# Kernel optimization log

Measured on AMD Instinct MI355X. Metric: run time of the kernel, lower is better.

Reference implementation:

```python
import jax, jax.numpy as jnp
import numpy as np

N, FIN, FOUT, H = 6144, 128, 64, 2
ALPHA = 0.2      # leaky relu slope
EPS = 1e-5       # layernorm eps
NEG = -9e15      # mask value from original code


def setup_inputs() -> dict:
    key = jax.random.key(0)
    k1, k2, k3, k4 = jax.random.split(key, 4)
    h = jax.random.normal(k1, (N, FIN), dtype=jnp.float32)
    adj = jax.random.randint(k2, (N, N), 0, 2, dtype=jnp.int32)
    # xavier_uniform over (fan_in, fan_out) of last two dims
    limW = float(np.sqrt(6.0 / (FIN + FOUT)))
    W = jax.random.uniform(k3, (H, FIN, FOUT), jnp.float32, -limW, limW)
    lima = float(np.sqrt(6.0 / (2 * FOUT + 1)))
    a = jax.random.uniform(k4, (H, 2 * FOUT, 1), jnp.float32, -lima, lima)
    gamma = jnp.ones((H * FOUT,), jnp.float32)
    beta = jnp.zeros((H * FOUT,), jnp.float32)
    return {"h": h, "adj": adj, "W": W, "a": a, "gamma": gamma, "beta": beta}


def reference(h, adj, W, a, gamma, beta):
    # h: [N, Fin], adj: [N, N] int, W: [H, Fin, Fout], a: [H, 2*Fout, 1]
    ht = jnp.einsum('ni,hio->hno', h, W)          # [H, N, Fout]
    a1 = a[:, :FOUT, 0]                            # [H, Fout]
    a2 = a[:, FOUT:, 0]                            # [H, Fout]
    # concat score a^T [h_i || h_j] == s1_i + s2_j (identical math, no NxNx2F tensor)
    s1 = jnp.einsum('hno,ho->hn', ht, a1)          # [H, N]
    s2 = jnp.einsum('hno,ho->hn', ht, a2)          # [H, N]
    e = s1[:, :, None] + s2[:, None, :]            # [H, N, N]
    e = jnp.where(e > 0, e, ALPHA * e)             # LeakyReLU
    e = jnp.where((adj > 0)[None], e, NEG)         # adjacency mask
    att = jax.nn.softmax(e, axis=-1)               # softmax over neighbors (dim=1 of [N,N])
    # dropout is identity in eval mode
    hp = jnp.einsum('hnm,hmo->hno', att, ht)       # [H, N, Fout]
    out = jnp.transpose(hp, (1, 0, 2)).reshape(N, H * FOUT)  # concat heads
    # LayerNorm(H*Fout), elementwise affine
    mu = out.mean(-1, keepdims=True)
    var = ((out - mu) ** 2).mean(-1, keepdims=True)
    out = (out - mu) / jnp.sqrt(var + EPS) * gamma + beta
    return out, att
```

## Files before the change

### kernel.cpp

```cpp
#include <hip/hip_runtime.h>
#include <hip/hip_bf16.h>

#define NNODES 6144
#define FIN    128
#define FOUTC  64
#define NHEAD  2
#define ALPHA  0.2f
#define LN_EPS 1e-5f
#define MASKW  192

typedef __attribute__((ext_vector_type(4))) float f32x4;
typedef __attribute__((ext_vector_type(8))) short short8;
typedef __attribute__((ext_vector_type(4))) int   i32x4;

static __device__ __forceinline__ short f2bf(float x) {
    unsigned u = __float_as_uint(x);
    u = (u + 0x7fffu + ((u >> 16) & 1u)) >> 16;
    return (short)u;
}

static __device__ __forceinline__ short f2bf_hw(float x) {
    return (short)__bfloat16_as_ushort(__float2bfloat16(x));
}

static __device__ __forceinline__ float pcalc(float s1v, float s2v, unsigned bit,
                                              bool uni, float inv) {
    float e = s1v + s2v;
    e = fmaxf(e, ALPHA * e);
    float t = bit ? __expf(e) : 0.0f;
    t = uni ? 1.0f : t;
    return t * inv;
}

static __device__ __forceinline__ float ecalc(float s1v, float s2v, int am) {
    float e = s1v + s2v;
    e = fmaxf(e, ALPHA * e);
    return (am > 0) ? __expf(e) : 0.0f;
}

static __device__ __forceinline__ float tcalc(float s1v, float s2v, unsigned bit,
                                              bool uni) {
    float e = s1v + s2v;
    e = fmaxf(e, ALPHA * e);
    float t = bit ? __expf(e) : 0.0f;
    return uni ? 1.0f : t;
}

__global__ __launch_bounds__(256) void gat_k1(const float* __restrict__ h,
        const float* __restrict__ W, const float* __restrict__ a,
        short* __restrict__ htbP, float* __restrict__ s1, float* __restrict__ s2) {
    __shared__ float hrow[4][FIN];
    const int wid = threadIdx.x >> 6, lane = threadIdx.x & 63;
    const int n = blockIdx.x * 4 + wid;
    hrow[wid][lane]      = h[(size_t)n * FIN + lane];
    hrow[wid][lane + 64] = h[(size_t)n * FIN + lane + 64];
    __syncthreads();
    float acc0 = 0.f, acc1 = 0.f;
    #pragma unroll 8
    for (int k = 0; k < FIN; ++k) {
        float hv = hrow[wid][k];
        acc0 = fmaf(hv, W[k * FOUTC + lane], acc0);
        acc1 = fmaf(hv, W[(FIN + k) * FOUTC + lane], acc1);
    }
    const int it_ = n >> 5, kk = n & 31;
    const int fl  = (lane & 15) + ((kk >> 3) << 4);
    const size_t pb = ((size_t)(it_ * 4 + (lane >> 4))) * 512 + fl * 8 + (kk & 7);
    htbP[pb]          = f2bf(acc0);
    htbP[393216 + pb] = f2bf(acc1);
    float r00 = acc0 * a[lane];
    float r01 = acc0 * a[FOUTC + lane];
    float r10 = acc1 * a[2 * FOUTC + lane];
    float r11 = acc1 * a[3 * FOUTC + lane];
    #pragma unroll
    for (int off = 32; off; off >>= 1) {
        r00 += __shfl_xor(r00, off);
        r01 += __shfl_xor(r01, off);
        r10 += __shfl_xor(r10, off);
        r11 += __shfl_xor(r11, off);
    }
    if (lane == 0) {
        s1[n] = r00;          s2[n] = r01;
        s1[NNODES + n] = r10; s2[NNODES + n] = r11;
    }
}

__global__ __launch_bounds__(256) void gat_k2a(const int* __restrict__ adj,
        const float* __restrict__ s1, const float* __restrict__ s2,
        float* __restrict__ psum, unsigned* __restrict__ mask32) {
    const int n = blockIdx.x;
    const int t = threadIdx.x;
    const int wid = t >> 6, lane = t & 63;
    const i32x4* arow = (const i32x4*)(adj + (size_t)n * NNODES);
    const float4* s2h0 = (const float4*)(s2);
    const float4* s2h1 = (const float4*)(s2 + NNODES);
    const float s10 = s1[n], s11 = s1[NNODES + n];
    float sum0 = 0.f, sum1 = 0.f;
    unsigned* mrow = mask32 + (size_t)n * MASKW;
    #pragma unroll
    for (int i = 0; i < 6; ++i) {
        int c4 = t + i * 256;
        i32x4 av = __builtin_nontemporal_load(arow + c4);
        float4 sa = s2h0[c4];
        float4 sb = s2h1[c4];
        sum0 += (ecalc(s10, sa.x, av[0]) + ecalc(s10, sa.y, av[1]))
              + (ecalc(s10, sa.z, av[2]) + ecalc(s10, sa.w, av[3]));
        sum1 += (ecalc(s11, sb.x, av[0]) + ecalc(s11, sb.y, av[1]))
              + (ecalc(s11, sb.z, av[2]) + ecalc(s11, sb.w, av[3]));
        unsigned nib = (unsigned)(av[0] > 0) | ((unsigned)(av[1] > 0) << 1)
                     | ((unsigned)(av[2] > 0) << 2) | ((unsigned)(av[3] > 0) << 3);
        unsigned v = nib << ((lane & 7) * 4);
        v |= (unsigned)__shfl_xor((int)v, 1);
        v |= (unsigned)__shfl_xor((int)v, 2);
        v |= (unsigned)__shfl_xor((int)v, 4);
        if ((lane & 7) == 0)
            mrow[i * 32 + wid * 8 + (lane >> 3)] = v;
    }
    #pragma unroll
    for (int off = 32; off; off >>= 1) {
        sum0 += __shfl_xor(sum0, off);
        sum1 += __shfl_xor(sum1, off);
    }
    __shared__ float red[2][4];
    if (lane == 0) { red[0][wid] = sum0; red[1][wid] = sum1; }
    __syncthreads();
    if (t == 0) {
        psum[n]          = (red[0][0] + red[0][1]) + (red[0][2] + red[0][3]);
        psum[NNODES + n] = (red[1][0] + red[1][1]) + (red[1][2] + red[1][3]);
    }
}

template <int ITERS, int RATIO>
__global__ __launch_bounds__(256) void gat_mixed(const unsigned* __restrict__ mask32,
        const short* __restrict__ htbP, const float* __restrict__ s1,
        const float* __restrict__ s2, const float* __restrict__ psum,
        float* __restrict__ att, float* __restrict__ hpp) {
    const int bid = blockIdx.x;
    const int mid = bid / RATIO, rem = bid % RATIO;

    if (rem == RATIO - 1) {
        const int bx = (6144 / ITERS / 32 == 4) ? (mid & 1) : 0;
        const int by = (6144 / ITERS / 32 == 4) ? (mid >> 1) : mid;
        const int w = threadIdx.x >> 6, lane = threadIdx.x & 63;
        const int hh = w & 1, cs = w >> 1;
        const int pc = bx * 2 + cs;
        const int n0 = by * 16;
        const int r = lane & 15, g = lane >> 4;
        const int node = n0 + r;
        const float s1v = s1[hh * NNODES + node];
        const float ps  = psum[hh * NNODES + node];
        const bool uni = !(ps > 0.f);
        const float* s2h = s2 + hh * NNODES;
        const unsigned* mrow = mask32 + (size_t)node * MASKW + pc * ITERS;
        const short* bb = htbP + (size_t)(hh * 192 + pc * ITERS) * 2048 + (size_t)lane * 8;
        const int cbase = pc * ITERS * 32;

        f32x4 acc0 = {0.f,0.f,0.f,0.f}, acc1 = {0.f,0.f,0.f,0.f};
        f32x4 acc2 = {0.f,0.f,0.f,0.f}, acc3 = {0.f,0.f,0.f,0.f};

        #pragma unroll 4
        for (int it = 0; it < ITERS; ++it) {
            const int kb = cbase + it * 32 + g * 8;
            const unsigned mb = (mrow[it] >> (g * 8)) & 0xffu;
            float4 sa = *(const float4*)(s2h + kb);
            float4 sb = *(const float4*)(s2h + kb + 4);
            float t0 = tcalc(s1v, sa.x, mb & 1u,   uni);
            float t1 = tcalc(s1v, sa.y, mb & 2u,   uni);
            float t2 = tcalc(s1v, sa.z, mb & 4u,   uni);
            float t3 = tcalc(s1v, sa.w, mb & 8u,   uni);
            float t4 = tcalc(s1v, sb.x, mb & 16u,  uni);
            float t5 = tcalc(s1v, sb.y, mb & 32u,  uni);
            float t6 = tcalc(s1v, sb.z, mb & 64u,  uni);
            float t7 = tcalc(s1v, sb.w, mb & 128u, uni);
            short8 af = { f2bf_hw(t0), f2bf_hw(t1), f2bf_hw(t2), f2bf_hw(t3),
                          f2bf_hw(t4), f2bf_hw(t5), f2bf_hw(t6), f2bf_hw(t7) };
            const short* bp = bb + (size_t)it * 2048;
            short8 b0 = *(const short8*)(bp);
            short8 b1 = *(const short8*)(bp + 512);
            short8 b2 = *(const short8*)(bp + 1024);
            short8 b3 = *(const short8*)(bp + 1536);
            acc0 = __builtin_amdgcn_mfma_f32_16x16x32_bf16(af, b0, acc0, 0, 0, 0);
            acc1 = __builtin_amdgcn_mfma_f32_16x16x32_bf16(af, b1, acc1, 0, 0, 0);
            acc2 = __builtin_amdgcn_mfma_f32_16x16x32_bf16(af, b2, acc2, 0, 0, 0);
            acc3 = __builtin_amdgcn_mfma_f32_16x16x32_bf16(af, b3, acc3, 0, 0, 0);
        }
        float invO[4];
        #pragma unroll
        for (int reg = 0; reg < 4; ++reg) {
            float pso = psum[hh * NNODES + n0 + g * 4 + reg];
            invO[reg] = (pso > 0.f) ? (1.0f / pso) : (1.0f / (float)NNODES);
        }
        float* hb = hpp + ((size_t)(pc * NHEAD + hh) * NNODES + (n0 + g * 4)) * FOUTC + r;
        #pragma unroll
        for (int reg = 0; reg < 4; ++reg) {
            hb[(size_t)reg * FOUTC +  0] = acc0[reg] * invO[reg];
            hb[(size_t)reg * FOUTC + 16] = acc1[reg] * invO[reg];
            hb[(size_t)reg * FOUTC + 32] = acc2[reg] * invO[reg];
            hb[(size_t)reg * FOUTC + 48] = acc3[reg] * invO[reg];
        }
    } else {
        const int row = mid * (RATIO - 1) + rem;
        const int t = threadIdx.x;
        const float ps0 = psum[row],          ps1 = psum[NNODES + row];
        const bool u0 = !(ps0 > 0.f),         u1 = !(ps1 > 0.f);
        const float in0 = u0 ? (1.0f / (float)NNODES) : 1.0f / ps0;
        const float in1 = u1 ? (1.0f / (float)NNODES) : 1.0f / ps1;
        const float s10 = s1[row], s11 = s1[NNODES + row];
        const unsigned* mrow = mask32 + (size_t)row * MASKW;
        float* attr0 = att + (size_t)row * NNODES;
        float* attr1 = attr0 + (size_t)NNODES * NNODES;
        const int sh = (t & 7) * 4;
        #pragma unroll
        for (int i = 0; i < 6; ++i) {
            const int c0 = i * 1024 + t * 4;
            const unsigned bits = (mrow[c0 >> 5] >> sh) & 0xfu;
            float4 sv0 = *(const float4*)(s2 + c0);
            float4 sv1 = *(const float4*)(s2 + NNODES + c0);
            f32x4 st0 = { pcalc(s10, sv0.x, bits & 1u, u0, in0),
                          pcalc(s10, sv0.y, bits & 2u, u0, in0),
                          pcalc(s10, sv0.z, bits & 4u, u0, in0),
                          pcalc(s10, sv0.w, bits & 8u, u0, in0) };
            f32x4 st1 = { pcalc(s11, sv1.x, bits & 1u, u1, in1),
                          pcalc(s11, sv1.y, bits & 2u, u1, in1),
                          pcalc(s11, sv1.z, bits & 4u, u1, in1),
                          pcalc(s11, sv1.w, bits & 8u, u1, in1) };
            __builtin_nontemporal_store(st0, (f32x4*)(attr0 + c0));
            __builtin_nontemporal_store(st1, (f32x4*)(attr1 + c0));
        }
    }
}

__global__ __launch_bounds__(256) void gat_k4(const float* __restrict__ hpp,
        const float* __restrict__ gamma, const float* __restrict__ beta,
        float* __restrict__ out, int nchunk) {
    const int wid = threadIdx.x >> 6, lane = threadIdx.x & 63;
    const int n = blockIdx.x * 4 + wid;
    float v0 = 0.f, v1 = 0.f;
    for (int p = 0; p < nchunk; ++p) {
        v0 += hpp[((size_t)(p * NHEAD + 0) * NNODES + n) * FOUTC + lane];
        v1 += hpp[((size_t)(p * NHEAD + 1) * NNODES + n) * FOUTC + lane];
    }
    float s = v0 + v1;
    #pragma unroll
    for (int off = 32; off; off >>= 1) s += __shfl_xor(s, off);
    const float mu = s * (1.0f / 128.0f);
    const float d0 = v0 - mu, d1 = v1 - mu;
    float q = d0 * d0 + d1 * d1;
    #pragma unroll
    for (int off = 32; off; off >>= 1) q += __shfl_xor(q, off);
    const float rstd = 1.0f / sqrtf(q * (1.0f / 128.0f) + LN_EPS);
    out[(size_t)n * 128 + lane]      = d0 * rstd * gamma[lane] + beta[lane];
    out[(size_t)n * 128 + 64 + lane] = d1 * rstd * gamma[64 + lane] + beta[64 + lane];
}

extern "C" void kernel_launch(void* const* d_in, const int* in_sizes, int n_in,
                              void* d_out, int out_size, void* d_ws, size_t ws_size,
                              hipStream_t stream) {
    const float* h     = (const float*)d_in[0];
    const int*   adj   = (const int*)d_in[1];
    const float* W     = (const float*)d_in[2];
    const float* a     = (const float*)d_in[3];
    const float* gamma = (const float*)d_in[4];
    const float* beta  = (const float*)d_in[5];
    float* out = (float*)d_out;
    float* att = out + (size_t)NNODES * (NHEAD * FOUTC);

    char* ws = (char*)d_ws;
    short* htbP = (short*)ws;
    float* s1   = (float*)(ws + 1572864);
    float* s2p  = (float*)(ws + 1572864 + 49152);
    float* psum = (float*)(ws + 1572864 + 2 * 49152);
    unsigned* mask32 = (unsigned*)(ws + 1572864 + 3 * 49152);
    char* hpp_base = ws + 1572864 + 3 * 49152 + 4718592;
    size_t avail = (ws_size > 6438912) ? ws_size - 6438912 : 0;
    const size_t per_chunk = (size_t)NHEAD * NNODES * FOUTC * 4;
    const int nchunk = (avail >= 4 * per_chunk) ? 4 : 2;
    float* hpp = (float*)hpp_base;

    gat_k1<<<NNODES / 4, 256, 0, stream>>>(h, W, a, htbP, s1, s2p);
    gat_k2a<<<NNODES, 256, 0, stream>>>(adj, s1, s2p, psum, mask32);
    if (nchunk == 4) {
        gat_mixed<48, 9><<<6912, 256, 0, stream>>>(mask32, htbP, s1, s2p, psum, att, hpp);
    } else {
        gat_mixed<96, 17><<<6528, 256, 0, stream>>>(mask32, htbP, s1, s2p, psum, att, hpp);
    }
    gat_k4<<<NNODES / 4, 256, 0, stream>>>(hpp, gamma, beta, out, nchunk);
}
```

Measured before the change: 139.0 us.

## Fold softmax normalization into exp2 exponent and split attention rows per head

Scores are pre-scaled by log2(e) so exp2 can be used directly, and the 1/sum normalization is folded into the exponent as -log2(psum). The MFMA path now accumulates already-normalized probabilities, so the output rescale loop is removed. Attention-writer blocks now handle one head-row each instead of both heads, which doubles the grid and changes RATIO. Fully masked rows take a fast path that just stores the uniform value. Normalizing inside the exponent changes bf16 rounding of the MFMA operands slightly.

Measured after the change: 140.0 us. No clear change (+0.7%).

```diff
diff --git a/kernel.cpp b/kernel.cpp
--- a/kernel.cpp
+++ b/kernel.cpp
@@ -8,6 +8,8 @@
 #define ALPHA  0.2f
 #define LN_EPS 1e-5f
 #define MASKW  192
+#define LOG2E  1.4426950408889634f
+#define INVN   (1.0f / 6144.0f)
 
 typedef __attribute__((ext_vector_type(4))) float f32x4;
 typedef __attribute__((ext_vector_type(8))) short short8;
@@ -23,27 +25,15 @@
     return (short)__bfloat16_as_ushort(__float2bfloat16(x));
 }
 
-static __device__ __forceinline__ float pcalc(float s1v, float s2v, unsigned bit,
-                                              bool uni, float inv) {
-    float e = s1v + s2v;
-    e = fmaxf(e, ALPHA * e);
-    float t = bit ? __expf(e) : 0.0f;
-    t = uni ? 1.0f : t;
-    return t * inv;
-}
-
-static __device__ __forceinline__ float ecalc(float s1v, float s2v, int am) {
-    float e = s1v + s2v;
-    e = fmaxf(e, ALPHA * e);
-    return (am > 0) ? __expf(e) : 0.0f;
-}
-
-static __device__ __forceinline__ float tcalc(float s1v, float s2v, unsigned bit,
-                                              bool uni) {
-    float e = s1v + s2v;
-    e = fmaxf(e, ALPHA * e);
-    float t = bit ? __expf(e) : 0.0f;
-    return uni ? 1.0f : t;
+static __device__ __forceinline__ float ecalc2(float e, unsigned bit) {
+    float m = fmaxf(e, ALPHA * e);
+    return bit ? __builtin_amdgcn_exp2f(m) : 0.0f;
+}
+static __device__ __forceinline__ float pcalc2(float e, float li, unsigned bit,
+                                               bool uni) {
+    float m = fmaxf(e, ALPHA * e) + li;
+    float t = bit ? __builtin_amdgcn_exp2f(m) : 0.0f;
+    return uni ? INVN : t;
 }
 
 __global__ __launch_bounds__(256) void gat_k1(const float* __restrict__ h,
@@ -79,8 +69,8 @@
         r11 += __shfl_xor(r11, off);
     }
     if (lane == 0) {
-        s1[n] = r00;          s2[n] = r01;
-        s1[NNODES + n] = r10; s2[NNODES + n] = r11;
+        s1[n] = r00 * LOG2E;          s2[n] = r01 * LOG2E;
+        s1[NNODES + n] = r10 * LOG2E; s2[NNODES + n] = r11 * LOG2E;
     }
 }
 
@@ -102,12 +92,12 @@
         i32x4 av = __builtin_nontemporal_load(arow + c4);
         float4 sa = s2h0[c4];
         float4 sb = s2h1[c4];
-        sum0 += (ecalc(s10, sa.x, av[0]) + ecalc(s10, sa.y, av[1]))
-              + (ecalc(s10, sa.z, av[2]) + ecalc(s10, sa.w, av[3]));
-        sum1 += (ecalc(s11, sb.x, av[0]) + ecalc(s11, sb.y, av[1]))
-              + (ecalc(s11, sb.z, av[2]) + ecalc(s11, sb.w, av[3]));
         unsigned nib = (unsigned)(av[0] > 0) | ((unsigned)(av[1] > 0) << 1)
                      | ((unsigned)(av[2] > 0) << 2) | ((unsigned)(av[3] > 0) << 3);
+        sum0 += (ecalc2(s10 + sa.x, nib & 1u) + ecalc2(s10 + sa.y, nib & 2u))
+              + (ecalc2(s10 + sa.z, nib & 4u) + ecalc2(s10 + sa.w, nib & 8u));
+        sum1 += (ecalc2(s11 + sb.x, nib & 1u) + ecalc2(s11 + sb.y, nib & 2u))
+              + (ecalc2(s11 + sb.z, nib & 4u) + ecalc2(s11 + sb.w, nib & 8u));
         unsigned v = nib << ((lane & 7) * 4);
         v |= (unsigned)__shfl_xor((int)v, 1);
         v |= (unsigned)__shfl_xor((int)v, 2);
@@ -149,6 +139,7 @@
         const float s1v = s1[hh * NNODES + node];
         const float ps  = psum[hh * NNODES + node];
         const bool uni = !(ps > 0.f);
+        const float li = uni ? 0.f : -__log2f(ps);
         const float* s2h = s2 + hh * NNODES;
         const unsigned* mrow = mask32 + (size_t)node * MASKW + pc * ITERS;
         const short* bb = htbP + (size_t)(hh * 192 + pc * ITERS) * 2048 + (size_t)lane * 8;
@@ -163,16 +154,16 @@
             const unsigned mb = (mrow[it] >> (g * 8)) & 0xffu;
             float4 sa = *(const float4*)(s2h + kb);
             float4 sb = *(const float4*)(s2h + kb + 4);
-            float t0 = tcalc(s1v, sa.x, mb & 1u,   uni);
-            float t1 = tcalc(s1v, sa.y, mb & 2u,   uni);
-            float t2 = tcalc(s1v, sa.z, mb & 4u,   uni);
-            float t3 = tcalc(s1v, sa.w, mb & 8u,   uni);
-            float t4 = tcalc(s1v, sb.x, mb & 16u,  uni);
-            float t5 = tcalc(s1v, sb.y, mb & 32u,  uni);
-            float t6 = tcalc(s1v, sb.z, mb & 64u,  uni);
-            float t7 = tcalc(s1v, sb.w, mb & 128u, uni);
-            short8 af = { f2bf_hw(t0), f2bf_hw(t1), f2bf_hw(t2), f2bf_hw(t3),
-                          f2bf_hw(t4), f2bf_hw(t5), f2bf_hw(t6), f2bf_hw(t7) };
+            float p0 = pcalc2(s1v + sa.x, li, mb & 1u,   uni);
+            float p1 = pcalc2(s1v + sa.y, li, mb & 2u,   uni);
+            float p2 = pcalc2(s1v + sa.z, li, mb & 4u,   uni);
+            float p3 = pcalc2(s1v + sa.w, li, mb & 8u,   uni);
+            float p4 = pcalc2(s1v + sb.x, li, mb & 16u,  uni);
+            float p5 = pcalc2(s1v + sb.y, li, mb & 32u,  uni);
+            float p6 = pcalc2(s1v + sb.z, li, mb & 64u,  uni);
+            float p7 = pcalc2(s1v + sb.w, li, mb & 128u, uni);
+            short8 af = { f2bf_hw(p0), f2bf_hw(p1), f2bf_hw(p2), f2bf_hw(p3),
+                          f2bf_hw(p4), f2bf_hw(p5), f2bf_hw(p6), f2bf_hw(p7) };
             const short* bp = bb + (size_t)it * 2048;
             short8 b0 = *(const short8*)(bp);
             short8 b1 = *(const short8*)(bp + 512);
@@ -183,48 +174,43 @@
             acc2 = __builtin_amdgcn_mfma_f32_16x16x32_bf16(af, b2, acc2, 0, 0, 0);
             acc3 = __builtin_amdgcn_mfma_f32_16x16x32_bf16(af, b3, acc3, 0, 0, 0);
         }
-        float invO[4];
-        #pragma unroll
-        for (int reg = 0; reg < 4; ++reg) {
-            float pso = psum[hh * NNODES + n0 + g * 4 + reg];
-            invO[reg] = (pso > 0.f) ? (1.0f / pso) : (1.0f / (float)NNODES);
-        }
         float* hb = hpp + ((size_t)(pc * NHEAD + hh) * NNODES + (n0 + g * 4)) * FOUTC + r;
         #pragma unroll
         for (int reg = 0; reg < 4; ++reg) {
-            hb[(size_t)reg * FOUTC +  0] = acc0[reg] * invO[reg];
-            hb[(size_t)reg * FOUTC + 16] = acc1[reg] * invO[reg];
-            hb[(size_t)reg * FOUTC + 32] = acc2[reg] * invO[reg];
-            hb[(size_t)reg * FOUTC + 48] = acc3[reg] * invO[reg];
+            hb[(size_t)reg * FOUTC +  0] = acc0[reg];
+            hb[(size_t)reg * FOUTC + 16] = acc1[reg];
+            hb[(size_t)reg * FOUTC + 32] = acc2[reg];
+            hb[(size_t)reg * FOUTC + 48] = acc3[reg];
         }
     } else {
-        const int row = mid * (RATIO - 1) + rem;
+        const int idx = mid * (RATIO - 1) + rem;
+        const int hh  = idx / NNODES;
+        const int row = idx - hh * NNODES;
         const int t = threadIdx.x;
-        const float ps0 = psum[row],          ps1 = psum[NNODES + row];
-        const bool u0 = !(ps0 > 0.f),         u1 = !(ps1 > 0.f);
-        const float in0 = u0 ? (1.0f / (float)NNODES) : 1.0f / ps0;
-        const float in1 = u1 ? (1.0f / (float)NNODES) : 1.0f / ps1;
-        const float s10 = s1[row], s11 = s1[NNODES + row];
+        const float ps = psum[hh * NNODES + row];
+        float* attrow = att + ((size_t)hh * NNODES + row) * NNODES;
+        if (!(ps > 0.f)) {
+            const f32x4 u = {INVN, INVN, INVN, INVN};
+            #pragma unroll
+            for (int i = 0; i < 6; ++i)
+                __builtin_nontemporal_store(u, (f32x4*)(attrow + i * 1024 + t * 4));
+            return;
+        }
+        const float li = -__log2f(ps);
+        const float s1v = s1[hh * NNODES + row];
+        const float* s2h = s2 + hh * NNODES;
         const unsigned* mrow = mask32 + (size_t)row * MASKW;
-        float* attr0 = att + (size_t)row * NNODES;
-        float* attr1 = attr0 + (size_t)NNODES * NNODES;
         const int sh = (t & 7) * 4;
         #pragma unroll
         for (int i = 0; i < 6; ++i) {
             const int c0 = i * 1024 + t * 4;
             const unsigned bits = (mrow[c0 >> 5] >> sh) & 0xfu;
-            float4 sv0 = *(const float4*)(s2 + c0);
-            float4 sv1 = *(const float4*)(s2 + NNODES + c0);
-            f32x4 st0 = { pcalc(s10, sv0.x, bits & 1u, u0, in0),
-                          pcalc(s10, sv0.y, bits & 2u, u0, in0),
-                          pcalc(s10, sv0.z, bits & 4u, u0, in0),
-                          pcalc(s10, sv0.w, bits & 8u, u0, in0) };
-            f32x4 st1 = { pcalc(s11, sv1.x, bits & 1u, u1, in1),
-                          pcalc(s11, sv1.y, bits & 2u, u1, in1),
-                          pcalc(s11, sv1.z, bits & 4u, u1, in1),
-                          pcalc(s11, sv1.w, bits & 8u, u1, in1) };
-            __builtin_nontemporal_store(st0, (f32x4*)(attr0 + c0));
-            __builtin_nontemporal_store(st1, (f32x4*)(attr1 + c0));
+            float4 sv = *(const float4*)(s2h + c0);
+            f32x4 st = { pcalc2(s1v + sv.x, li, bits & 1u, false),
+                         pcalc2(s1v + sv.y, li, bits & 2u, false),
+                         pcalc2(s1v + sv.z, li, bits & 4u, false),
+                         pcalc2(s1v + sv.w, li, bits & 8u, false) };
+            __builtin_nontemporal_store(st, (f32x4*)(attrow + c0));
         }
     }
 }
@@ -279,9 +265,9 @@
     gat_k1<<<NNODES / 4, 256, 0, stream>>>(h, W, a, htbP, s1, s2p);
     gat_k2a<<<NNODES, 256, 0, stream>>>(adj, s1, s2p, psum, mask32);
     if (nchunk == 4) {
-        gat_mixed<48, 9><<<6912, 256, 0, stream>>>(mask32, htbP, s1, s2p, psum, att, hpp);
+        gat_mixed<48, 17><<<13056, 256, 0, stream>>>(mask32, htbP, s1, s2p, psum, att, hpp);
     } else {
-        gat_mixed<96, 17><<<6528, 256, 0, stream>>>(mask32, htbP, s1, s2p, psum, att, hpp);
+        gat_mixed<96, 33><<<12672, 256, 0, stream>>>(mask32, htbP, s1, s2p, psum, att, hpp);
     }
     gat_k4<<<NNODES / 4, 256, 0, stream>>>(hpp, gamma, beta, out, nchunk);
 }
```
